# Kernel tuning notes

Measured on AMD Instinct MI355X. Metric: run time of the kernel, lower is better.

The kernel has to match this reference:

```python
import jax, jax.numpy as jnp
import numpy as np

NUM_HEADS = 12
ATTN_BALANCE = 0.3
ROPE_THETA = 10000.0
EPS = 1e-4


def _mp_weight(w):
    # Eval-mode MPConv weight prep: per-output-channel magnitude-preserving
    # normalize (normalize() with alpha=sqrt(1/fan_in)), then scale by gain/sqrt(fan_in).
    O = w.shape[0]
    fan = int(np.prod(w.shape[1:]))  # in_channels * 1 * 1
    wf = w.astype(jnp.float32).reshape(O, -1)
    n = jnp.linalg.norm(wf, axis=1, keepdims=True)
    wn = wf / (EPS + n / np.sqrt(fan))
    return wn / np.sqrt(fan)  # [O, fan]; 1x1 kernel -> acts as a dense matrix


def _normalize_lastdim(x):
    # normalize(y, dim=-1): denom = eps + ||x||_2 * sqrt(1/c)
    c = x.shape[-1]
    n = jnp.linalg.norm(x.astype(jnp.float32), axis=-1, keepdims=True)
    return x / (EPS + n / np.sqrt(c)).astype(x.dtype)


def _rope(q, k):
    c = q.shape[-1]
    t = q.shape[2]
    inv_freq = 1.0 / (ROPE_THETA ** (jnp.arange(0, c, 2, dtype=jnp.float32) / c))  # [c/2]
    ang = jnp.arange(t, dtype=jnp.float32)[:, None] * inv_freq                      # [t, c/2]
    cos = jnp.cos(ang)[None, None, :, None, :]
    sin = jnp.sin(ang)[None, None, :, None, :]

    def rot(x):
        x1, x2 = jnp.split(x, 2, axis=-1)
        return jnp.concatenate([x1 * cos - x2 * sin, x2 * cos + x1 * sin], axis=-1)

    return rot(q), rot(k)


def setup_inputs() -> dict:
    key = jax.random.key(0)
    k1, k2, k3 = jax.random.split(key, 3)
    B, C, H, W = 32, 768, 16, 16  # B = batch_size * n_frames = 2 * 16
    x = jax.random.normal(k1, (B, C, H, W), dtype=jnp.float32)
    w_qkv = jax.random.normal(k2, (3 * C, C, 1, 1), dtype=jnp.float32)
    w_proj = jax.random.normal(k3, (C, C, 1, 1), dtype=jnp.float32)
    return {"x": x, "w_qkv": w_qkv, "w_proj": w_proj, "batch_size": 2}


def reference(x, w_qkv, w_proj, batch_size):
    B, C, H, W = x.shape
    m = NUM_HEADS
    c = C // m
    t = B // batch_size
    i = H * W
    T = t * i

    wq = _mp_weight(w_qkv).astype(x.dtype)   # [3C, C]
    wp = _mp_weight(w_proj).astype(x.dtype)  # [C, C]

    # 1x1 conv == channel matmul
    y = jnp.einsum('bchw,oc->bohw', x, wq)
    # '(b t) (s m c) h w -> b s m t (h w) c'
    y = y.reshape(batch_size, t, 3, m, c, i).transpose(0, 2, 3, 1, 5, 4)  # [b,3,m,t,i,c]
    y = _normalize_lastdim(y)
    q, k, v = y[:, 0], y[:, 1], y[:, 2]  # each [b, m, t, i, c]
    q, k = _rope(q, k)

    q = q.reshape(batch_size, m, T, c)
    k = k.reshape(batch_size, m, T, c)
    v = v.reshape(batch_size, m, T, c)

    # frame-causal block mask: q_frame >= kv_frame (infer-mode mask of the module)
    scores = jnp.einsum('bmqc,bmkc->bmqk', q, k) / np.sqrt(c)
    frame = jnp.arange(T) // i
    mask = frame[:, None] >= frame[None, :]  # [T, T] bool, block structure over frames
    scores = jnp.where(mask, scores, -jnp.inf)
    attn = jax.nn.softmax(scores, axis=-1)
    o = jnp.einsum('bmqk,bmkc->bmqc', attn, v)

    # 'b m (t h w) c -> (b t) (c m) h w'  (channel index = c_idx * m + m_idx)
    o = o.reshape(batch_size, m, t, H, W, c).transpose(0, 2, 5, 1, 3, 4).reshape(B, C, H, W)
    o = jnp.einsum('bchw,oc->bohw', o, wp)

    tt = ATTN_BALANCE  # mp_sum(x, o, t)
    return (x + tt * (o - x)) / np.sqrt((1.0 - tt) ** 2 + tt ** 2)
```

## Files before the change

### kernel.cpp

```cpp
#include <hip/hip_runtime.h>
#include <hip/hip_bf16.h>
#include <math.h>

typedef __hip_bfloat16 bf16;
typedef __attribute__((ext_vector_type(8))) short short8;
typedef __attribute__((ext_vector_type(4))) float f32x4;

#define EPSV 0.0001f

__device__ __forceinline__ unsigned short f2bf(float f) {
    unsigned int u = __float_as_uint(f);
    u += 0x7fff + ((u >> 16) & 1);
    return (unsigned short)(u >> 16);
}
__device__ __forceinline__ unsigned int pkbf(float a, float b) {
    __hip_bfloat162 h = __float22bfloat162_rn(make_float2(a, b));
    return *(unsigned int*)&h;
}
__device__ __forceinline__ float fast_exp2(float x) {
    return __builtin_amdgcn_exp2f(x);
}

__global__ __launch_bounds__(256) void rownorm_cast_kernel(
    const float* __restrict__ w_qkv, const float* __restrict__ w_proj,
    unsigned short* __restrict__ Wqb, unsigned short* __restrict__ Wpb)
{
    const int row = blockIdx.x;
    const float* src;
    unsigned short* dst;
    if (row < 2304) { src = w_qkv + (size_t)row * 768;           dst = Wqb + (size_t)row * 768; }
    else            { src = w_proj + (size_t)(row - 2304) * 768; dst = Wpb + (size_t)(row - 2304) * 768; }

    const int tid = threadIdx.x;
    float v[3];
    float ss = 0.f;
    #pragma unroll
    for (int j = 0; j < 3; j++) {
        v[j] = src[tid + j * 256];
        ss += v[j] * v[j];
    }
    #pragma unroll
    for (int off = 32; off > 0; off >>= 1) ss += __shfl_down(ss, off, 64);
    __shared__ float wsum[4];
    if ((tid & 63) == 0) wsum[tid >> 6] = ss;
    __syncthreads();
    const float total = wsum[0] + wsum[1] + wsum[2] + wsum[3];
    const float scale = 1.0f / (EPSV * 27.712812921102035f + sqrtf(total));
    #pragma unroll
    for (int j = 0; j < 3; j++) dst[tid + j * 256] = f2bf(v[j] * scale);
}

__global__ __launch_bounds__(256) void cast_x_kernel(
    const float* __restrict__ X, unsigned short* __restrict__ XbT)
{
    const int c0 = blockIdx.x * 64;
    const int b  = blockIdx.y;
    const int pos = threadIdx.x;
    const float* src = X + ((size_t)b * 768 + c0) * 256 + pos;
    unsigned short* dst = XbT + ((size_t)b * 256 + pos) * 768 + c0;
    #pragma unroll
    for (int cc = 0; cc < 8; cc++) {
        short8 t;
        #pragma unroll
        for (int j = 0; j < 8; j++)
            t[j] = (short)f2bf(src[(size_t)(cc * 8 + j) * 256]);
        *(short8*)&dst[cc * 8] = t;
    }
}

__global__ __launch_bounds__(256, 2) void qkv_mfma_kernel(
    const unsigned short* __restrict__ Wqb,
    const unsigned short* __restrict__ XbT,
    bf16* __restrict__ Q, bf16* __restrict__ K, bf16* __restrict__ Vt)
{
    const int g = blockIdx.x;
    const int b = blockIdx.y;
    const int bs = b >> 4, fr = b & 15;
    const int qkv = g / 12, head = g % 12;
    const int m0 = g * 64;

    const int tid = threadIdx.x;
    const int w = tid >> 6, lane = tid & 63;
    const int l15 = lane & 15, quad = lane >> 4;

    __shared__ unsigned short As[64 * 72];
    __shared__ unsigned short Bs[256 * 72];

    const unsigned short* Ag = Wqb + (size_t)m0 * 768;
    const unsigned short* Bg = XbT + (size_t)b * 256 * 768;

    f32x4 acc[4][4];
    #pragma unroll
    for (int mi = 0; mi < 4; mi++)
        #pragma unroll
        for (int ni = 0; ni < 4; ni++)
            acc[mi][ni] = (f32x4){0.f, 0.f, 0.f, 0.f};

    const int arow = tid >> 2, acol = (tid & 3) * 16;
    const int brow = tid >> 3, bcol = (tid & 7) * 8;

    for (int k0 = 0; k0 < 768; k0 += 64) {
        const short8 av0 = *(const short8*)&Ag[(size_t)arow * 768 + k0 + acol];
        const short8 av1 = *(const short8*)&Ag[(size_t)arow * 768 + k0 + acol + 8];
        short8 bv[8];
        #pragma unroll
        for (int p = 0; p < 8; p++)
            bv[p] = *(const short8*)&Bg[(size_t)(32 * p + brow) * 768 + k0 + bcol];
        __syncthreads();
        *(short8*)&As[arow * 72 + acol] = av0;
        *(short8*)&As[arow * 72 + acol + 8] = av1;
        #pragma unroll
        for (int p = 0; p < 8; p++)
            *(short8*)&Bs[(32 * p + brow) * 72 + bcol] = bv[p];
        __syncthreads();

        short8 af[4][2], bfr[4][2];
        #pragma unroll
        for (int mi = 0; mi < 4; mi++)
            #pragma unroll
            for (int kk = 0; kk < 2; kk++)
                af[mi][kk] = *(const short8*)&As[(16 * mi + l15) * 72 + 32 * kk + 8 * quad];
        #pragma unroll
        for (int ni = 0; ni < 4; ni++)
            #pragma unroll
            for (int kk = 0; kk < 2; kk++)
                bfr[ni][kk] = *(const short8*)&Bs[(64 * w + 16 * ni + l15) * 72 + 32 * kk + 8 * quad];
        #pragma unroll
        for (int kk = 0; kk < 2; kk++)
            #pragma unroll
            for (int mi = 0; mi < 4; mi++)
                #pragma unroll
                for (int ni = 0; ni < 4; ni++)
                    acc[mi][ni] = __builtin_amdgcn_mfma_f32_16x16x32_bf16(af[mi][kk], bfr[ni][kk], acc[mi][ni], 0, 0, 0);
    }

    float inv[4];
    #pragma unroll
    for (int ni = 0; ni < 4; ni++) {
        float ssq = 0.f;
        #pragma unroll
        for (int mi = 0; mi < 4; mi++)
            #pragma unroll
            for (int r = 0; r < 4; r++)
                ssq = fmaf(acc[mi][ni][r], acc[mi][ni][r], ssq);
        ssq += __shfl_xor(ssq, 16, 64);
        ssq += __shfl_xor(ssq, 32, 64);
        inv[ni] = 1.0f / (EPSV + sqrtf(ssq) * 0.125f);
    }

    if (qkv == 2) {
        unsigned short* Vb = &Bs[w * 64 * 72];
        #pragma unroll
        for (int ni = 0; ni < 4; ni++)
            #pragma unroll
            for (int mi = 0; mi < 4; mi++) {
                uint2 d;
                d.x = pkbf(acc[mi][ni][0] * inv[ni], acc[mi][ni][1] * inv[ni]);
                d.y = pkbf(acc[mi][ni][2] * inv[ni], acc[mi][ni][3] * inv[ni]);
                *(uint2*)&Vb[(16 * ni + l15) * 72 + 16 * mi + 4 * quad] = d;
            }
        unsigned short* Vtu = (unsigned short*)Vt;
        const size_t cb = ((size_t)(bs * 12 + head) * 64);
        const int tok = fr * 256 + 64 * w + lane;
        #pragma unroll 8
        for (int ch = 0; ch < 64; ch++)
            Vtu[(cb + ch) * 4096 + tok] = Vb[lane * 72 + ch];
    } else {
        unsigned short* dst = (unsigned short*)((qkv == 0) ? Q : K);
        const float post = (qkv == 0) ? 0.125f : 1.0f;
        #pragma unroll
        for (int ni = 0; ni < 4; ni++) {
            const int token = fr * 256 + 64 * w + 16 * ni + l15;
            const size_t base = (((size_t)(bs * 12 + head)) * 4096 + token) * 64;
            #pragma unroll
            for (int mi = 0; mi < 2; mi++) {
                unsigned int lo[2], hi[2];
                #pragma unroll
                for (int r = 0; r < 4; r++) {
                    const int j = 16 * mi + 4 * quad + r;
                    const float n1 = acc[mi][ni][r] * inv[ni];
                    const float n2 = acc[mi + 2][ni][r] * inv[ni];
                    const float ang = (float)fr * exp2f(-(float)j * 0.41524101186092029f);
                    float sn, cs;
                    __sincosf(ang, &sn, &cs);
                    const unsigned short o1 = f2bf((n1 * cs - n2 * sn) * post);
                    const unsigned short o2 = f2bf((n2 * cs + n1 * sn) * post);
                    if (r < 2) { if (r == 0) { lo[0] = o1; hi[0] = o2; } else { lo[0] |= (unsigned int)o1 << 16; hi[0] |= (unsigned int)o2 << 16; } }
                    else       { if (r == 2) { lo[1] = o1; hi[1] = o2; } else { lo[1] |= (unsigned int)o1 << 16; hi[1] |= (unsigned int)o2 << 16; } }
                }
                *(uint2*)&dst[base + 16 * mi + 4 * quad]      = make_uint2(lo[0], lo[1]);
                *(uint2*)&dst[base + 32 + 16 * mi + 4 * quad] = make_uint2(hi[0], hi[1]);
            }
        }
    }
}

__global__ __launch_bounds__(256, 3) void attn_mfma_kernel(
    const bf16* __restrict__ Qg, const bf16* __restrict__ Kg,
    const bf16* __restrict__ Vtg, unsigned short* __restrict__ OspT)
{
    const int px = blockIdx.x;
    const int p = px >> 2, sub = px & 3;
    const int fa = p, fb = 15 - p;
    const int head = blockIdx.y, bs = blockIdx.z;
    const int tid = threadIdx.x;
    const int w = tid >> 6, lane = tid & 63;
    const int l15 = lane & 15, quad = lane >> 4;
    const size_t hb = ((size_t)(bs * 12 + head)) * 4096 * 64;

    __shared__ unsigned short Ks[64 * 72];
    __shared__ unsigned short Vs[64 * 72];
    __shared__ unsigned short Pw[4][2][16 * 72];

    const unsigned short* Qu = (const unsigned short*)Qg;
    const unsigned short* Ku = (const unsigned short*)Kg;
    const unsigned short* Vu = (const unsigned short*)Vtg;

    short8 Qfa[2], Qfb[2];
    {
        const int qra = fa * 256 + sub * 64 + w * 16 + l15;
        const int qrb = fb * 256 + sub * 64 + w * 16 + l15;
        #pragma unroll
        for (int kk = 0; kk < 2; kk++) {
            Qfa[kk] = *(const short8*)&Qu[hb + (size_t)qra * 64 + 32 * kk + 8 * quad];
            Qfb[kk] = *(const short8*)&Qu[hb + (size_t)qrb * 64 + 32 * kk + 8 * quad];
        }
    }

    f32x4 Oa[4], Ob[4];
    #pragma unroll
    for (int c = 0; c < 4; c++) {
        Oa[c] = (f32x4){0.f, 0.f, 0.f, 0.f};
        Ob[c] = (f32x4){0.f, 0.f, 0.f, 0.f};
    }
    float la = 0.f, lb = 0.f;
    const f32x4 zf = (f32x4){0.f, 0.f, 0.f, 0.f};
    const float L2E = 1.4426950408889634f;
    const float C = 11.541560327111707f;

    const int stage_row = tid >> 2;
    const int stage_off = (tid & 3) * 16;
    const unsigned short* Kst = Ku + hb + stage_off;
    const unsigned short* Vst = Vu + hb + (size_t)stage_row * 4096 + stage_off;

    short8 ka = *(const short8*)&Kst[(size_t)stage_row * 64];
    short8 kb = *(const short8*)&Kst[(size_t)stage_row * 64 + 8];
    short8 va = *(const short8*)&Vst[0];
    short8 vb = *(const short8*)&Vst[8];

    const int nka = (fa + 1) * 256;
    const int nkb = (fb + 1) * 256;
    for (int t0 = 0; t0 < nkb; t0 += 64) {
        __syncthreads();
        *(short8*)&Ks[stage_row * 72 + stage_off] = ka;
        *(short8*)&Ks[stage_row * 72 + stage_off + 8] = kb;
        *(short8*)&Vs[stage_row * 72 + stage_off] = va;
        *(short8*)&Vs[stage_row * 72 + stage_off + 8] = vb;
        __syncthreads();

        const int tn = (t0 + 64 < nkb) ? t0 + 64 : t0;
        ka = *(const short8*)&Kst[(size_t)(tn + stage_row) * 64];
        kb = *(const short8*)&Kst[(size_t)(tn + stage_row) * 64 + 8];
        va = *(const short8*)&Vst[tn];
        vb = *(const short8*)&Vst[tn + 8];

        const bool doA = (t0 < nka);

        f32x4 Sa[4], Sb[4];
        #pragma unroll
        for (int mi = 0; mi < 4; mi++) {
            const short8 kf0 = *(const short8*)&Ks[(16 * mi + l15) * 72 + 8 * quad];
            const short8 kf1 = *(const short8*)&Ks[(16 * mi + l15) * 72 + 32 + 8 * quad];
            f32x4 s = __builtin_amdgcn_mfma_f32_16x16x32_bf16(kf0, Qfb[0], zf, 0, 0, 0);
            Sb[mi] = __builtin_amdgcn_mfma_f32_16x16x32_bf16(kf1, Qfb[1], s, 0, 0, 0);
            if (doA) {
                f32x4 sa = __builtin_amdgcn_mfma_f32_16x16x32_bf16(kf0, Qfa[0], zf, 0, 0, 0);
                Sa[mi] = __builtin_amdgcn_mfma_f32_16x16x32_bf16(kf1, Qfa[1], sa, 0, 0, 0);
            }
        }

        #pragma unroll
        for (int mi = 0; mi < 4; mi++) {
            const f32x4 s = Sb[mi];
            const float p0 = fast_exp2(fmaf(s[0], L2E, -C));
            const float p1 = fast_exp2(fmaf(s[1], L2E, -C));
            const float p2 = fast_exp2(fmaf(s[2], L2E, -C));
            const float p3 = fast_exp2(fmaf(s[3], L2E, -C));
            lb += (p0 + p1) + (p2 + p3);
            uint2 d;
            d.x = pkbf(p0, p1);
            d.y = pkbf(p2, p3);
            *(uint2*)&Pw[w][1][l15 * 72 + 16 * mi + 4 * quad] = d;
        }
        if (doA) {
            #pragma unroll
            for (int mi = 0; mi < 4; mi++) {
                const f32x4 s = Sa[mi];
                const float p0 = fast_exp2(fmaf(s[0], L2E, -C));
                const float p1 = fast_exp2(fmaf(s[1], L2E, -C));
                const float p2 = fast_exp2(fmaf(s[2], L2E, -C));
                const float p3 = fast_exp2(fmaf(s[3], L2E, -C));
                la += (p0 + p1) + (p2 + p3);
                uint2 d;
                d.x = pkbf(p0, p1);
                d.y = pkbf(p2, p3);
                *(uint2*)&Pw[w][0][l15 * 72 + 16 * mi + 4 * quad] = d;
            }
        }

        short8 Pfb[2], Pfa[2];
        #pragma unroll
        for (int ks = 0; ks < 2; ks++)
            Pfb[ks] = *(const short8*)&Pw[w][1][l15 * 72 + 32 * ks + 8 * quad];
        if (doA) {
            #pragma unroll
            for (int ks = 0; ks < 2; ks++)
                Pfa[ks] = *(const short8*)&Pw[w][0][l15 * 72 + 32 * ks + 8 * quad];
        }

        #pragma unroll
        for (int ci = 0; ci < 4; ci++) {
            const short8 vf0 = *(const short8*)&Vs[(16 * ci + l15) * 72 + 8 * quad];
            const short8 vf1 = *(const short8*)&Vs[(16 * ci + l15) * 72 + 32 + 8 * quad];
            Ob[ci] = __builtin_amdgcn_mfma_f32_16x16x32_bf16(Pfb[0], vf0, Ob[ci], 0, 0, 0);
            Ob[ci] = __builtin_amdgcn_mfma_f32_16x16x32_bf16(Pfb[1], vf1, Ob[ci], 0, 0, 0);
            if (doA) {
                Oa[ci] = __builtin_amdgcn_mfma_f32_16x16x32_bf16(Pfa[0], vf0, Oa[ci], 0, 0, 0);
                Oa[ci] = __builtin_amdgcn_mfma_f32_16x16x32_bf16(Pfa[1], vf1, Oa[ci], 0, 0, 0);
            }
        }
    }

    la += __shfl_xor(la, 16, 64);
    la += __shfl_xor(la, 32, 64);
    la = 1.0f / la;
    lb += __shfl_xor(lb, 16, 64);
    lb += __shfl_xor(lb, 32, 64);
    lb = 1.0f / lb;

    const size_t oba = ((size_t)(bs * 16 + fa)) * 196608;
    const size_t obb = ((size_t)(bs * 16 + fb)) * 196608;
    #pragma unroll
    for (int r = 0; r < 4; r++) {
        const float ia = __shfl(la, quad * 4 + r, 64);
        const float ib = __shfl(lb, quad * 4 + r, 64);
        const int pos = sub * 64 + w * 16 + 4 * quad + r;
        #pragma unroll
        for (int ci = 0; ci < 4; ci++) {
            const int chan = (16 * ci + l15) * 12 + head;
            OspT[oba + (size_t)pos * 768 + chan] = f2bf(Oa[ci][r] * ia);
            OspT[obb + (size_t)pos * 768 + chan] = f2bf(Ob[ci][r] * ib);
        }
    }
}

__global__ __launch_bounds__(256, 2) void proj_mfma_kernel(
    const unsigned short* __restrict__ Wpb,
    const unsigned short* __restrict__ OspT,
    const float* __restrict__ X,
    float* __restrict__ Out)
{
    const int my = blockIdx.x;
    const int b  = blockIdx.y;
    const int m0 = my * 64;

    const int tid = threadIdx.x;
    const int w = tid >> 6, lane = tid & 63;
    const int l15 = lane & 15, quad = lane >> 4;

    __shared__ unsigned short As[64 * 72];
    __shared__ unsigned short Bs[256 * 72];

    const unsigned short* Ag = Wpb + (size_t)m0 * 768;
    const unsigned short* Bg = OspT + (size_t)b * 256 * 768;

    f32x4 acc[4][4];
    #pragma unroll
    for (int mi = 0; mi < 4; mi++)
        #pragma unroll
        for (int ni = 0; ni < 4; ni++)
            acc[mi][ni] = (f32x4){0.f, 0.f, 0.f, 0.f};

    const int arow = tid >> 2, acol = (tid & 3) * 16;
    const int brow = tid >> 3, bcol = (tid & 7) * 8;

    for (int k0 = 0; k0 < 768; k0 += 64) {
        const short8 av0 = *(const short8*)&Ag[(size_t)arow * 768 + k0 + acol];
        const short8 av1 = *(const short8*)&Ag[(size_t)arow * 768 + k0 + acol + 8];
        short8 bv[8];
        #pragma unroll
        for (int p = 0; p < 8; p++)
            bv[p] = *(const short8*)&Bg[(size_t)(32 * p + brow) * 768 + k0 + bcol];
        __syncthreads();
        *(short8*)&As[arow * 72 + acol] = av0;
        *(short8*)&As[arow * 72 + acol + 8] = av1;
        #pragma unroll
        for (int p = 0; p < 8; p++)
            *(short8*)&Bs[(32 * p + brow) * 72 + bcol] = bv[p];
        __syncthreads();

        short8 af[4][2], bfr[4][2];
        #pragma unroll
        for (int mi = 0; mi < 4; mi++)
            #pragma unroll
            for (int kk = 0; kk < 2; kk++)
                af[mi][kk] = *(const short8*)&As[(16 * mi + l15) * 72 + 32 * kk + 8 * quad];
        #pragma unroll
        for (int ni = 0; ni < 4; ni++)
            #pragma unroll
            for (int kk = 0; kk < 2; kk++)
                bfr[ni][kk] = *(const short8*)&Bs[(64 * w + 16 * ni + l15) * 72 + 32 * kk + 8 * quad];
        #pragma unroll
        for (int kk = 0; kk < 2; kk++)
            #pragma unroll
            for (int mi = 0; mi < 4; mi++)
                #pragma unroll
                for (int ni = 0; ni < 4; ni++)
                    acc[mi][ni] = __builtin_amdgcn_mfma_f32_16x16x32_bf16(af[mi][kk], bfr[ni][kk], acc[mi][ni], 0, 0, 0);
    }

    const float kMix = 1.3130643285972254f;
    #pragma unroll
    for (int mi = 0; mi < 4; mi++)
        #pragma unroll
        for (int r = 0; r < 4; r++) {
            const int m = m0 + 16 * mi + 4 * quad + r;
            const size_t rowb = (size_t)b * 196608 + (size_t)m * 256;
            #pragma unroll
            for (int ni = 0; ni < 4; ni++) {
                const int n = 64 * w + 16 * ni + l15;
                Out[rowb + n] = (0.7f * X[rowb + n] + 0.3f * acc[mi][ni][r]) * kMix;
            }
        }
}

extern "C" void kernel_launch(void* const* d_in, const int* in_sizes, int n_in,
                              void* d_out, int out_size, void* d_ws, size_t ws_size,
                              hipStream_t stream) {
    const float* x     = (const float*)d_in[0];
    const float* wqkv  = (const float*)d_in[1];
    const float* wproj = (const float*)d_in[2];
    float* out = (float*)d_out;

    char* ws = (char*)d_ws;
    unsigned short* Wqb  = (unsigned short*)(ws + 0);
    unsigned short* Wpb  = (unsigned short*)(ws + 3538944);
    unsigned short* XbT  = (unsigned short*)(ws + 4718592);
    unsigned short* OspT = XbT;
    bf16*  Q   = (bf16*)(ws + 17301504);
    bf16*  K   = (bf16*)(ws + 29884416);
    bf16*  Vt  = (bf16*)(ws + 42467328);

    rownorm_cast_kernel<<<3072, 256, 0, stream>>>(wqkv, wproj, Wqb, Wpb);
    cast_x_kernel<<<dim3(12, 32), 256, 0, stream>>>(x, XbT);
    qkv_mfma_kernel<<<dim3(36, 32), 256, 0, stream>>>(Wqb, XbT, Q, K, Vt);
    attn_mfma_kernel<<<dim3(32, 12, 2), 256, 0, stream>>>(Q, K, Vt, OspT);
    proj_mfma_kernel<<<dim3(12, 32), 256, 0, stream>>>(Wpb, OspT, x, out);
}
```

Before: 261.3 us.

## Split QK by key columns per wave, load K fragments directly from global

Each wave now computes scores for all 64 query rows of the block against its own 16-key slice, holding all four Q row-groups in registers and loading K fragments straight from global memory, which removes the K shared-memory staging buffer. Probabilities are written to a block-shared P tile and exchanged across waves with an extra barrier before the PV MFMA. Row sums are now taken from the bf16-rounded P fragments after reload. This cuts LDS traffic for K but raises register pressure (eight Q fragments per pair) and adds a block-wide sync per tile.

```diff
diff --git a/kernel.cpp b/kernel.cpp
--- a/kernel.cpp
+++ b/kernel.cpp
@@ -8,6 +8,9 @@
 
 #define EPSV 0.0001f
 
+__device__ __forceinline__ float bfbits2f(unsigned int u16) {
+    return __uint_as_float(u16 << 16);
+}
 __device__ __forceinline__ unsigned short f2bf(float f) {
     unsigned int u = __float_as_uint(f);
     u += 0x7fff + ((u >> 16) & 1);
@@ -208,22 +211,22 @@
     const int l15 = lane & 15, quad = lane >> 4;
     const size_t hb = ((size_t)(bs * 12 + head)) * 4096 * 64;
 
-    __shared__ unsigned short Ks[64 * 72];
     __shared__ unsigned short Vs[64 * 72];
-    __shared__ unsigned short Pw[4][2][16 * 72];
+    __shared__ unsigned short Pw[2][64 * 72];
 
     const unsigned short* Qu = (const unsigned short*)Qg;
     const unsigned short* Ku = (const unsigned short*)Kg;
     const unsigned short* Vu = (const unsigned short*)Vtg;
 
-    short8 Qfa[2], Qfb[2];
-    {
-        const int qra = fa * 256 + sub * 64 + w * 16 + l15;
-        const int qrb = fb * 256 + sub * 64 + w * 16 + l15;
+    short8 Qfa[4][2], Qfb[4][2];
+    #pragma unroll
+    for (int ni = 0; ni < 4; ni++) {
+        const int qra = fa * 256 + sub * 64 + 16 * ni + l15;
+        const int qrb = fb * 256 + sub * 64 + 16 * ni + l15;
         #pragma unroll
         for (int kk = 0; kk < 2; kk++) {
-            Qfa[kk] = *(const short8*)&Qu[hb + (size_t)qra * 64 + 32 * kk + 8 * quad];
-            Qfb[kk] = *(const short8*)&Qu[hb + (size_t)qrb * 64 + 32 * kk + 8 * quad];
+            Qfa[ni][kk] = *(const short8*)&Qu[hb + (size_t)qra * 64 + 32 * kk + 8 * quad];
+            Qfb[ni][kk] = *(const short8*)&Qu[hb + (size_t)qrb * 64 + 32 * kk + 8 * quad];
         }
     }
 
@@ -240,11 +243,9 @@
 
     const int stage_row = tid >> 2;
     const int stage_off = (tid & 3) * 16;
-    const unsigned short* Kst = Ku + hb + stage_off;
     const unsigned short* Vst = Vu + hb + (size_t)stage_row * 4096 + stage_off;
-
-    short8 ka = *(const short8*)&Kst[(size_t)stage_row * 64];
-    short8 kb = *(const short8*)&Kst[(size_t)stage_row * 64 + 8];
+    const unsigned short* Klane = Ku + hb + (size_t)(16 * w + l15) * 64 + 8 * quad;
+
     short8 va = *(const short8*)&Vst[0];
     short8 vb = *(const short8*)&Vst[8];
 
@@ -252,72 +253,76 @@
     const int nkb = (fb + 1) * 256;
     for (int t0 = 0; t0 < nkb; t0 += 64) {
         __syncthreads();
-        *(short8*)&Ks[stage_row * 72 + stage_off] = ka;
-        *(short8*)&Ks[stage_row * 72 + stage_off + 8] = kb;
+        const short8 kf0 = *(const short8*)&Klane[(size_t)t0 * 64];
+        const short8 kf1 = *(const short8*)&Klane[(size_t)t0 * 64 + 32];
         *(short8*)&Vs[stage_row * 72 + stage_off] = va;
         *(short8*)&Vs[stage_row * 72 + stage_off + 8] = vb;
         __syncthreads();
 
         const int tn = (t0 + 64 < nkb) ? t0 + 64 : t0;
-        ka = *(const short8*)&Kst[(size_t)(tn + stage_row) * 64];
-        kb = *(const short8*)&Kst[(size_t)(tn + stage_row) * 64 + 8];
         va = *(const short8*)&Vst[tn];
         vb = *(const short8*)&Vst[tn + 8];
 
         const bool doA = (t0 < nka);
 
-        f32x4 Sa[4], Sb[4];
-        #pragma unroll
-        for (int mi = 0; mi < 4; mi++) {
-            const short8 kf0 = *(const short8*)&Ks[(16 * mi + l15) * 72 + 8 * quad];
-            const short8 kf1 = *(const short8*)&Ks[(16 * mi + l15) * 72 + 32 + 8 * quad];
-            f32x4 s = __builtin_amdgcn_mfma_f32_16x16x32_bf16(kf0, Qfb[0], zf, 0, 0, 0);
-            Sb[mi] = __builtin_amdgcn_mfma_f32_16x16x32_bf16(kf1, Qfb[1], s, 0, 0, 0);
+        {
+            f32x4 St[4];
+            #pragma unroll
+            for (int ni = 0; ni < 4; ni++) {
+                f32x4 s = __builtin_amdgcn_mfma_f32_16x16x32_bf16(kf0, Qfb[ni][0], zf, 0, 0, 0);
+                St[ni] = __builtin_amdgcn_mfma_f32_16x16x32_bf16(kf1, Qfb[ni][1], s, 0, 0, 0);
+            }
+            #pragma unroll
+            for (int ni = 0; ni < 4; ni++) {
+                const f32x4 s = St[ni];
+                uint2 d;
+                d.x = pkbf(fast_exp2(fmaf(s[0], L2E, -C)), fast_exp2(fmaf(s[1], L2E, -C)));
+                d.y = pkbf(fast_exp2(fmaf(s[2], L2E, -C)), fast_exp2(fmaf(s[3], L2E, -C)));
+                *(uint2*)&Pw[1][(16 * ni + l15) * 72 + 16 * w + 4 * quad] = d;
+            }
             if (doA) {
-                f32x4 sa = __builtin_amdgcn_mfma_f32_16x16x32_bf16(kf0, Qfa[0], zf, 0, 0, 0);
-                Sa[mi] = __builtin_amdgcn_mfma_f32_16x16x32_bf16(kf1, Qfa[1], sa, 0, 0, 0);
-            }
-        }
-
-        #pragma unroll
-        for (int mi = 0; mi < 4; mi++) {
-            const f32x4 s = Sb[mi];
-            const float p0 = fast_exp2(fmaf(s[0], L2E, -C));
-            const float p1 = fast_exp2(fmaf(s[1], L2E, -C));
-            const float p2 = fast_exp2(fmaf(s[2], L2E, -C));
-            const float p3 = fast_exp2(fmaf(s[3], L2E, -C));
-            lb += (p0 + p1) + (p2 + p3);
-            uint2 d;
-            d.x = pkbf(p0, p1);
-            d.y = pkbf(p2, p3);
-            *(uint2*)&Pw[w][1][l15 * 72 + 16 * mi + 4 * quad] = d;
-        }
+                #pragma unroll
+                for (int ni = 0; ni < 4; ni++) {
+                    f32x4 s = __builtin_amdgcn_mfma_f32_16x16x32_bf16(kf0, Qfa[ni][0], zf, 0, 0, 0);
+                    St[ni] = __builtin_amdgcn_mfma_f32_16x16x32_bf16(kf1, Qfa[ni][1], s, 0, 0, 0);
+                }
+                #pragma unroll
+                for (int ni = 0; ni < 4; ni++) {
+                    const f32x4 s = St[ni];
+                    uint2 d;
+                    d.x = pkbf(fast_exp2(fmaf(s[0], L2E, -C)), fast_exp2(fmaf(s[1], L2E, -C)));
+                    d.y = pkbf(fast_exp2(fmaf(s[2], L2E, -C)), fast_exp2(fmaf(s[3], L2E, -C)));
+                    *(uint2*)&Pw[0][(16 * ni + l15) * 72 + 16 * w + 4 * quad] = d;
+                }
+            }
+        }
+        __syncthreads();
+
+        short8 Pfb[2], Pfa[2];
+        #pragma unroll
+        for (int ks = 0; ks < 2; ks++)
+            Pfb[ks] = *(const short8*)&Pw[1][(16 * w + l15) * 72 + 32 * ks + 8 * quad];
         if (doA) {
             #pragma unroll
-            for (int mi = 0; mi < 4; mi++) {
-                const f32x4 s = Sa[mi];
-                const float p0 = fast_exp2(fmaf(s[0], L2E, -C));
-                const float p1 = fast_exp2(fmaf(s[1], L2E, -C));
-                const float p2 = fast_exp2(fmaf(s[2], L2E, -C));
-                const float p3 = fast_exp2(fmaf(s[3], L2E, -C));
-                la += (p0 + p1) + (p2 + p3);
-                uint2 d;
-                d.x = pkbf(p0, p1);
-                d.y = pkbf(p2, p3);
-                *(uint2*)&Pw[w][0][l15 * 72 + 16 * mi + 4 * quad] = d;
-            }
-        }
-
-        short8 Pfb[2], Pfa[2];
-        #pragma unroll
-        for (int ks = 0; ks < 2; ks++)
-            Pfb[ks] = *(const short8*)&Pw[w][1][l15 * 72 + 32 * ks + 8 * quad];
+            for (int ks = 0; ks < 2; ks++)
+                Pfa[ks] = *(const short8*)&Pw[0][(16 * w + l15) * 72 + 32 * ks + 8 * quad];
+        }
+        #pragma unroll
+        for (int ks = 0; ks < 2; ks++) {
+            const unsigned int* ub = (const unsigned int*)&Pfb[ks];
+            #pragma unroll
+            for (int j = 0; j < 4; j++)
+                lb += bfbits2f(ub[j] & 0xffffu) + bfbits2f(ub[j] >> 16);
+        }
         if (doA) {
             #pragma unroll
-            for (int ks = 0; ks < 2; ks++)
-                Pfa[ks] = *(const short8*)&Pw[w][0][l15 * 72 + 32 * ks + 8 * quad];
-        }
-
+            for (int ks = 0; ks < 2; ks++) {
+                const unsigned int* ua = (const unsigned int*)&Pfa[ks];
+                #pragma unroll
+                for (int j = 0; j < 4; j++)
+                    la += bfbits2f(ua[j] & 0xffffu) + bfbits2f(ua[j] >> 16);
+            }
+        }
         #pragma unroll
         for (int ci = 0; ci < 4; ci++) {
             const short8 vf0 = *(const short8*)&Vs[(16 * ci + l15) * 72 + 8 * quad];
```

Measured after the change: 255.4 us. 2.3% less time.
